# Kernel tuning notes

Measured on AMD Instinct MI355X. Metric: run time of the kernel, lower is better.

The kernel has to match this reference:

```python
import jax, jax.numpy as jnp
import numpy as np


def setup_inputs() -> dict:
    key = jax.random.key(0)
    ks = jax.random.split(key, 6)
    B, F, C = 2048, 512, 64
    t_feat = jax.random.normal(ks[0], (B, F), dtype=jnp.float32)
    f_feat = jax.random.normal(ks[1], (B, F), dtype=jnp.float32)
    # proj Linear(F*F -> C); scale like torch default init (~1/sqrt(fan_in))
    W_proj = jax.random.normal(ks[2], (C, F * F), dtype=jnp.float32) / np.sqrt(F * F)
    b_proj = jnp.zeros((C,), dtype=jnp.float32)
    W1 = jax.random.normal(ks[3], (32, C), dtype=jnp.float32) / np.sqrt(C)
    b1 = jnp.zeros((32,), dtype=jnp.float32)
    W2 = jax.random.normal(ks[4], (1, 32), dtype=jnp.float32) / np.sqrt(32)
    b2 = jnp.zeros((1,), dtype=jnp.float32)
    return {"t_feat": t_feat, "f_feat": f_feat, "W_proj": W_proj, "b_proj": b_proj,
            "W1": W1, "b1": b1, "W2": W2, "b2": b2}


def reference(t_feat, f_feat, W_proj, b_proj, W1, b1, W2, b2):
    B, F = t_feat.shape
    C = W_proj.shape[0]
    # corr[b,i,j] = t[b,i] * f[b,j]; proj = corr_flat @ W_proj.T + b_proj.
    # Equivalent bilinear form computed WITHOUT materializing the (B,F,F) outer product:
    Wr = W_proj.reshape(C, F, F)            # W_proj[c, i*F + j] -> Wr[c,i,j]
    tmp = jnp.einsum('bi,cij->bcj', t_feat, Wr)   # (B, C, F)
    proj = jnp.einsum('bcj,bj->bc', tmp, f_feat) + b_proj  # (B, C)
    h = jax.nn.relu(proj)
    # GRL is identity in forward
    h2 = jax.nn.relu(h @ W1.T + b1)          # (B, 32)
    logit = h2 @ W2.T + b2                   # (B, 1)
    return logit
```

## Files before the change

kernel.cpp:

```cpp
#include <hip/hip_runtime.h>
#include <hip/hip_bf16.h>
#include <stdint.h>

#define BATCH 2048
#define FDIM 512
#define CDIM 64

typedef unsigned short ushort_t;
typedef __attribute__((ext_vector_type(8))) short short8;
typedef __attribute__((ext_vector_type(4))) float f32x4;

__device__ __forceinline__ ushort_t f2bf(float x) {
    union { float f; uint32_t u; } v; v.f = x;
    uint32_t u = v.u;
    uint32_t r = u + 0x7FFFu + ((u >> 16) & 1u);
    return (ushort_t)(r >> 16);
}
__device__ __forceinline__ float bf2f(ushort_t u) {
    union { float f; uint32_t v; } x; x.v = ((uint32_t)u) << 16; return x.f;
}

__global__ void convert_all_kernel(const float* __restrict__ W, ushort_t* __restrict__ Wb,
                                   const float* __restrict__ f, ushort_t* __restrict__ f16,
                                   const float* __restrict__ t, ushort_t* __restrict__ t16) {
    int blk = blockIdx.x;
    const float* src; ushort_t* dst; int idx;
    if (blk < 8192)      { src = W; dst = Wb;  idx = blk * 256 + threadIdx.x; }
    else if (blk < 8704) { src = f; dst = f16; idx = (blk - 8192) * 256 + threadIdx.x; }
    else                 { src = t; dst = t16; idx = (blk - 8704) * 256 + threadIdx.x; }
    float4 v0 = ((const float4*)src)[idx * 2];
    float4 v1 = ((const float4*)src)[idx * 2 + 1];
    ushort_t p[8] = { f2bf(v0.x), f2bf(v0.y), f2bf(v0.z), f2bf(v0.w),
                      f2bf(v1.x), f2bf(v1.y), f2bf(v1.z), f2bf(v1.w) };
    *(uint4*)&dst[idx * 8] = *(uint4*)p;
}

#define AS3(p) ((__attribute__((address_space(3))) void*)(p))
#define AS1(p) ((const __attribute__((address_space(1))) void*)(p))


#define STAGE(bi, kt)                                                               \
    __builtin_amdgcn_global_load_lds(AS1(gA0 + (kt) * 32), AS3(&As[bi][0 * 2048 + wave * 512]), 16, 0, 0); \
    __builtin_amdgcn_global_load_lds(AS1(gA1 + (kt) * 32), AS3(&As[bi][1 * 2048 + wave * 512]), 16, 0, 0); \
    __builtin_amdgcn_global_load_lds(AS1(gB0 + (kt) * 32), AS3(&Bs[bi][0 * 2048 + wave * 512]), 16, 0, 0); \
    __builtin_amdgcn_global_load_lds(AS1(gB1 + (kt) * 32), AS3(&Bs[bi][1 * 2048 + wave * 512]), 16, 0, 0);

#define COMPUTE(bi)                                                                 \
    { short8 a[4], b[4];                                                            \
      _Pragma("unroll")                                                             \
      for (int mi = 0; mi < 4; mi++) a[mi] = *(const short8*)&As[bi][a_off[mi]];    \
      _Pragma("unroll")                                                             \
      for (int ni = 0; ni < 4; ni++) b[ni] = *(const short8*)&Bs[bi][b_off[ni]];    \
      _Pragma("unroll")                                                             \
      for (int mi = 0; mi < 4; mi++) {                                              \
        _Pragma("unroll")                                                           \
        for (int ni = 0; ni < 4; ni++)                                              \
          acc[mi][ni] = __builtin_amdgcn_mfma_f32_16x16x32_bf16(                    \
              a[mi], b[ni], acc[mi][ni], 0, 0, 0);                                  \
      } }

__launch_bounds__(256, 4)
__global__ void gemm_fused_kernel(const ushort_t* __restrict__ f16,
                                  const ushort_t* __restrict__ Wb,
                                  const ushort_t* __restrict__ t16,
                                  float* __restrict__ part) {
    __shared__ ushort_t As[2][128 * 32];
    __shared__ ushort_t Bs[2][128 * 32];
    __shared__ float scratch[256];

    const int tid  = threadIdx.x;
    const int wave = tid >> 6;
    const int lane = tid & 63;
    const int l15  = lane & 15;
    const int lg   = lane >> 4;

    const int m_base = (wave >> 1) * 64;
    const int nh     = wave & 1;
    const int n_base = nh * 64;

    const int xcd = blockIdx.x & 7;
    const int idx = blockIdx.x >> 3;
    const int bx  = idx & 15;
    const int by  = xcd * 32 + (idx >> 4);
    const int b0  = bx * 128;
    const int n0  = by * 128;

    const int p    = tid >> 2;
    const int cph  = tid & 3;
    const int cg   = cph ^ ((p >> 1) & 3);
    const int nrot = ((p & 15) << 2) | (p >> 4);

    const ushort_t* gA0 = f16 + (size_t)(b0 + p) * FDIM + cg * 8;
    const ushort_t* gA1 = f16 + (size_t)(b0 + 64 + p) * FDIM + cg * 8;
    const ushort_t* gB0 = Wb + (size_t)(n0 + nrot) * FDIM + cg * 8;
    const ushort_t* gB1 = Wb + (size_t)(n0 + 64 + nrot) * FDIM + cg * 8;

    int a_off[4], b_off[4];
    #pragma unroll
    for (int mi = 0; mi < 4; mi++) {
        int r = m_base + mi * 16 + l15;
        a_off[mi] = r * 32 + (lg ^ ((r >> 1) & 3)) * 8;
    }
    #pragma unroll
    for (int ni = 0; ni < 4; ni++) {
        int q = n_base + ni * 16 + l15;
        b_off[ni] = q * 32 + (lg ^ ((q >> 1) & 3)) * 8;
    }

    f32x4 acc[4][4];
    #pragma unroll
    for (int mi = 0; mi < 4; mi++)
        #pragma unroll
        for (int ni = 0; ni < 4; ni++)
            acc[mi][ni] = (f32x4){0.f, 0.f, 0.f, 0.f};

    STAGE(0, 0)
    __syncthreads();
    #pragma unroll 1
    for (int t2 = 0; t2 < 7; t2++) {
        const int kt = t2 * 2;
        STAGE(1, kt + 1) COMPUTE(0) __syncthreads();
        STAGE(0, kt + 2) COMPUTE(1) __syncthreads();
    }
    STAGE(1, 15) COMPUTE(0) __syncthreads();
    COMPUTE(1)

    const int c  = n0 >> 9;
    const int iq = (n0 >> 7) & 3;
    const int i_base = (n0 & 511) + n_base + l15 * 4;

    #pragma unroll
    for (int mi = 0; mi < 4; mi++) {
        #pragma unroll
        for (int r = 0; r < 4; r++) {
            int b_idx = b0 + m_base + mi * 16 + lg * 4 + r;
            ushort4 tv = *(const ushort4*)&t16[(size_t)b_idx * FDIM + i_base];
            float sv = acc[mi][0][r] * bf2f(tv.x) + acc[mi][1][r] * bf2f(tv.y)
                     + acc[mi][2][r] * bf2f(tv.z) + acc[mi][3][r] * bf2f(tv.w);
            sv += __shfl_xor(sv, 1, 64);
            sv += __shfl_xor(sv, 2, 64);
            sv += __shfl_xor(sv, 4, 64);
            sv += __shfl_xor(sv, 8, 64);
            if (l15 == 0)
                scratch[(m_base + mi * 16 + lg * 4 + r) * 2 + nh] = sv;
        }
    }
    __syncthreads();
    if (tid < 128) {
        float v = scratch[tid * 2] + scratch[tid * 2 + 1];
        part[(((size_t)(b0 + tid)) * 64 + c) * 4 + iq] = v;
    }
}

__global__ void mlp_kernel(const float* __restrict__ part,
                           const float* __restrict__ b_proj,
                           const float* __restrict__ W1, const float* __restrict__ b1,
                           const float* __restrict__ W2, const float* __restrict__ b2,
                           float* __restrict__ out) {
    __shared__ float h[8][64];
    const int tid = threadIdx.x;
    const int bl  = tid >> 5;
    const int o   = tid & 31;
    const int b   = blockIdx.x * 8 + bl;

    #pragma unroll
    for (int c = o; c < 64; c += 32) {
        float4 v = *(const float4*)&part[(((size_t)b * 64 + c)) * 4];
        float sv = v.x + v.y + v.z + v.w + b_proj[c];
        h[bl][c] = sv > 0.f ? sv : 0.f;
    }
    __syncthreads();

    float sv = b1[o];
    #pragma unroll
    for (int c = 0; c < 64; c++) sv += h[bl][c] * W1[o * 64 + c];
    float v = (sv > 0.f ? sv : 0.f) * W2[o];
    v += __shfl_xor(v, 1, 32);
    v += __shfl_xor(v, 2, 32);
    v += __shfl_xor(v, 4, 32);
    v += __shfl_xor(v, 8, 32);
    v += __shfl_xor(v, 16, 32);
    if (o == 0) out[b] = v + b2[0];
}

extern "C" void kernel_launch(void* const* d_in, const int* in_sizes, int n_in,
                              void* d_out, int out_size, void* d_ws, size_t ws_size,
                              hipStream_t stream) {
    const float* t_feat = (const float*)d_in[0];
    const float* f_feat = (const float*)d_in[1];
    const float* W_proj = (const float*)d_in[2];
    const float* b_proj = (const float*)d_in[3];
    const float* W1     = (const float*)d_in[4];
    const float* b1     = (const float*)d_in[5];
    const float* W2     = (const float*)d_in[6];
    const float* b2     = (const float*)d_in[7];
    float* out = (float*)d_out;

    uint8_t* ws = (uint8_t*)d_ws;
    ushort_t* Wb   = (ushort_t*)(ws);
    ushort_t* f16  = (ushort_t*)(ws + 33554432);
    ushort_t* t16  = (ushort_t*)(ws + 33554432 + 2097152);
    float*    part = (float*)(ws + 33554432 + 2 * 2097152);

    convert_all_kernel<<<dim3(9216), dim3(256), 0, stream>>>(W_proj, Wb, f_feat, f16, t_feat, t16);

    gemm_fused_kernel<<<dim3((BATCH / 128) * ((CDIM * FDIM) / 128)), dim3(256), 0, stream>>>(
        f16, Wb, t16, part);

    mlp_kernel<<<dim3(BATCH / 8), dim3(256), 0, stream>>>(part, b_proj, W1, b1, W2, b2, out);
}
```

Baseline: 209.6 us.

## Enlarge GEMM block tile to 256x256 with 16 waves per block

The fused GEMM block grows from 128x128 with 4 waves to 256x256 with 16 waves (1024 threads), so each block stages twice the rows of A and B per k-step and global traffic per output drops. The cross-wave reduction now sums four N-waves, and the partial buffer holds two halves per channel instead of four, with the MLP kernel updated to match. The cost is higher LDS use per block (about 68 KB), fewer blocks resident per CU, and heavier barriers across 16 waves. The swizzle now uses the lane index instead of the row, which agrees because row offsets are multiples of 16.

```diff
diff --git a/kernel.cpp b/kernel.cpp
--- a/kernel.cpp
+++ b/kernel.cpp
@@ -40,10 +40,8 @@
 
 
 #define STAGE(bi, kt)                                                               \
-    __builtin_amdgcn_global_load_lds(AS1(gA0 + (kt) * 32), AS3(&As[bi][0 * 2048 + wave * 512]), 16, 0, 0); \
-    __builtin_amdgcn_global_load_lds(AS1(gA1 + (kt) * 32), AS3(&As[bi][1 * 2048 + wave * 512]), 16, 0, 0); \
-    __builtin_amdgcn_global_load_lds(AS1(gB0 + (kt) * 32), AS3(&Bs[bi][0 * 2048 + wave * 512]), 16, 0, 0); \
-    __builtin_amdgcn_global_load_lds(AS1(gB1 + (kt) * 32), AS3(&Bs[bi][1 * 2048 + wave * 512]), 16, 0, 0);
+    __builtin_amdgcn_global_load_lds(AS1(gA + (kt) * 32), AS3(&As[bi][wave * 512]), 16, 0, 0); \
+    __builtin_amdgcn_global_load_lds(AS1(gB + (kt) * 32), AS3(&Bs[bi][wave * 512]), 16, 0, 0);
 
 #define COMPUTE(bi)                                                                 \
     { short8 a[4], b[4];                                                            \
@@ -59,53 +57,47 @@
               a[mi], b[ni], acc[mi][ni], 0, 0, 0);                                  \
       } }
 
-__launch_bounds__(256, 4)
+__launch_bounds__(1024, 4)
 __global__ void gemm_fused_kernel(const ushort_t* __restrict__ f16,
                                   const ushort_t* __restrict__ Wb,
                                   const ushort_t* __restrict__ t16,
                                   float* __restrict__ part) {
-    __shared__ ushort_t As[2][128 * 32];
-    __shared__ ushort_t Bs[2][128 * 32];
-    __shared__ float scratch[256];
+    __shared__ ushort_t As[2][256 * 32];
+    __shared__ ushort_t Bs[2][256 * 32];
+    __shared__ float scratch[256 * 4];
 
     const int tid  = threadIdx.x;
     const int wave = tid >> 6;
     const int lane = tid & 63;
     const int l15  = lane & 15;
     const int lg   = lane >> 4;
-
-    const int m_base = (wave >> 1) * 64;
-    const int nh     = wave & 1;
-    const int n_base = nh * 64;
+    const int wm   = wave >> 2;
+    const int wn   = wave & 3;
+    const int m_base = wm * 64;
+    const int n_base = wn * 64;
 
     const int xcd = blockIdx.x & 7;
     const int idx = blockIdx.x >> 3;
-    const int bx  = idx & 15;
-    const int by  = xcd * 32 + (idx >> 4);
-    const int b0  = bx * 128;
-    const int n0  = by * 128;
+    const int bx  = idx & 7;
+    const int by  = xcd * 16 + (idx >> 3);
+    const int b0  = bx * 256;
+    const int n0  = by * 256;
 
     const int p    = tid >> 2;
     const int cph  = tid & 3;
     const int cg   = cph ^ ((p >> 1) & 3);
-    const int nrot = ((p & 15) << 2) | (p >> 4);
-
-    const ushort_t* gA0 = f16 + (size_t)(b0 + p) * FDIM + cg * 8;
-    const ushort_t* gA1 = f16 + (size_t)(b0 + 64 + p) * FDIM + cg * 8;
-    const ushort_t* gB0 = Wb + (size_t)(n0 + nrot) * FDIM + cg * 8;
-    const ushort_t* gB1 = Wb + (size_t)(n0 + 64 + nrot) * FDIM + cg * 8;
+    const int nrot = (p & 192) | ((p & 15) << 2) | ((p >> 4) & 3);
+
+    const ushort_t* gA = f16 + (size_t)(b0 + p) * FDIM + cg * 8;
+    const ushort_t* gB = Wb + (size_t)(n0 + nrot) * FDIM + cg * 8;
 
     int a_off[4], b_off[4];
     #pragma unroll
-    for (int mi = 0; mi < 4; mi++) {
-        int r = m_base + mi * 16 + l15;
-        a_off[mi] = r * 32 + (lg ^ ((r >> 1) & 3)) * 8;
-    }
-    #pragma unroll
-    for (int ni = 0; ni < 4; ni++) {
-        int q = n_base + ni * 16 + l15;
-        b_off[ni] = q * 32 + (lg ^ ((q >> 1) & 3)) * 8;
-    }
+    for (int mi = 0; mi < 4; mi++)
+        a_off[mi] = (m_base + mi * 16 + l15) * 32 + (lg ^ ((l15 >> 1) & 3)) * 8;
+    #pragma unroll
+    for (int ni = 0; ni < 4; ni++)
+        b_off[ni] = (n_base + ni * 16 + l15) * 32 + (lg ^ ((l15 >> 1) & 3)) * 8;
 
     f32x4 acc[4][4];
     #pragma unroll
@@ -125,8 +117,8 @@
     STAGE(1, 15) COMPUTE(0) __syncthreads();
     COMPUTE(1)
 
-    const int c  = n0 >> 9;
-    const int iq = (n0 >> 7) & 3;
+    const int c    = n0 >> 9;
+    const int half = (n0 >> 8) & 1;
     const int i_base = (n0 & 511) + n_base + l15 * 4;
 
     #pragma unroll
@@ -142,13 +134,13 @@
             sv += __shfl_xor(sv, 4, 64);
             sv += __shfl_xor(sv, 8, 64);
             if (l15 == 0)
-                scratch[(m_base + mi * 16 + lg * 4 + r) * 2 + nh] = sv;
+                scratch[(m_base + mi * 16 + lg * 4 + r) * 4 + wn] = sv;
         }
     }
     __syncthreads();
-    if (tid < 128) {
-        float v = scratch[tid * 2] + scratch[tid * 2 + 1];
-        part[(((size_t)(b0 + tid)) * 64 + c) * 4 + iq] = v;
+    if (tid < 256) {
+        float4 s4 = *(const float4*)&scratch[tid * 4];
+        part[((size_t)(b0 + tid) * CDIM + c) * 2 + half] = s4.x + s4.y + s4.z + s4.w;
     }
 }
 
@@ -165,8 +157,8 @@
 
     #pragma unroll
     for (int c = o; c < 64; c += 32) {
-        float4 v = *(const float4*)&part[(((size_t)b * 64 + c)) * 4];
-        float sv = v.x + v.y + v.z + v.w + b_proj[c];
+        float2 v = *(const float2*)&part[((size_t)b * 64 + c) * 2];
+        float sv = v.x + v.y + b_proj[c];
         h[bl][c] = sv > 0.f ? sv : 0.f;
     }
     __syncthreads();
@@ -204,8 +196,7 @@
 
     convert_all_kernel<<<dim3(9216), dim3(256), 0, stream>>>(W_proj, Wb, f_feat, f16, t_feat, t16);
 
-    gemm_fused_kernel<<<dim3((BATCH / 128) * ((CDIM * FDIM) / 128)), dim3(256), 0, stream>>>(
-        f16, Wb, t16, part);
+    gemm_fused_kernel<<<dim3(1024), dim3(1024), 0, stream>>>(f16, Wb, t16, part);
 
     mlp_kernel<<<dim3(BATCH / 8), dim3(256), 0, stream>>>(part, b_proj, W1, b1, W2, b2, out);
 }
```

After: 205.4 us. 2.0% less time.
